# Performance work log

Measured on AMD Instinct MI355X. Metric: run time of the kernel, lower is better.

Reference implementation:

```python
import jax, jax.numpy as jnp
import numpy as np

DIM = 1024
HEADS = 16
HEAD_DIM = DIM // HEADS
B, N = 2, 2048


def setup_inputs() -> dict:
    key = jax.random.key(0)
    k1, k2, k3, k4 = jax.random.split(key, 4)
    scale = 1.0 / np.sqrt(DIM)
    return {
        "x": jax.random.normal(k1, (B, N, DIM), dtype=jnp.float32),
        "w_qkv": jax.random.normal(k2, (DIM, 3 * DIM), dtype=jnp.float32) * scale,
        "w_out": jax.random.normal(k3, (DIM, DIM), dtype=jnp.float32) * scale,
        "b_out": jax.random.normal(k4, (DIM,), dtype=jnp.float32) * 0.01,
    }


def reference(x, w_qkv, w_out, b_out):
    b, n, c = x.shape
    h, d = HEADS, c // HEADS
    sm_scale = d ** -0.5
    qkv = x @ w_qkv  # [b, n, 3c]
    q, k, v = jnp.split(qkv, 3, axis=-1)
    # [b, n, c] -> [b, h, n, d]
    q = q.reshape(b, n, h, d).transpose(0, 2, 1, 3)
    k = k.reshape(b, n, h, d).transpose(0, 2, 1, 3)
    v = v.reshape(b, n, h, d).transpose(0, 2, 1, 3)
    dots = jnp.einsum("bhqd,bhkd->bhqk", q, k) * sm_scale
    attn = jax.nn.softmax(dots, axis=-1)
    out = jnp.einsum("bhqk,bhkd->bhqd", attn, v)
    out = out.transpose(0, 2, 1, 3).reshape(b, n, c)
    return out @ w_out + b_out
```

## Files before the change

### kernel.cpp

```cpp
#include <hip/hip_runtime.h>
#include <hip/hip_bf16.h>

typedef __attribute__((ext_vector_type(8))) short bf16x8;
typedef __attribute__((ext_vector_type(4))) float f32x4;

#define B_    2
#define N_    2048
#define DIM_  1024
#define H_    16
#define D_    64
#define BH_   32
#define QSC   0.18033688f

static __device__ __forceinline__ void gload_lds16(const void* g, void* l) {
  __builtin_amdgcn_global_load_lds((const __attribute__((address_space(1))) void*)g,
                                   (__attribute__((address_space(3))) void*)l, 16, 0, 0);
}

__global__ __launch_bounds__(256) void cvt_x_kernel(const float* __restrict__ in,
                                                    __hip_bfloat16* __restrict__ out, int n4) {
  int i = blockIdx.x * 256 + threadIdx.x;
  if (i >= n4) return;
  float4 v = reinterpret_cast<const float4*>(in)[i];
  union { __hip_bfloat16 h[4]; uint2 u; } cv;
  cv.h[0] = __float2bfloat16(v.x);
  cv.h[1] = __float2bfloat16(v.y);
  cv.h[2] = __float2bfloat16(v.z);
  cv.h[3] = __float2bfloat16(v.w);
  reinterpret_cast<uint2*>(out)[i] = cv.u;
}

__global__ __launch_bounds__(256) void tconv_kernel(const float* __restrict__ in,
                                                    __hip_bfloat16* __restrict__ out,
                                                    int R, int C) {
  __shared__ float tile[64][65];
  const int c0 = blockIdx.x * 64, r0 = blockIdx.y * 64;
  const int t = threadIdx.x;
#pragma unroll
  for (int i = 0; i < 16; ++i) {
    int idx = i * 256 + t;
    int r = idx >> 6, c = idx & 63;
    tile[r][c] = in[(size_t)(r0 + r) * C + (c0 + c)];
  }
  __syncthreads();
#pragma unroll
  for (int i = 0; i < 16; ++i) {
    int idx = i * 256 + t;
    int rr = idx >> 6, cc = idx & 63;
    out[(size_t)(c0 + rr) * R + (r0 + cc)] = __float2bfloat16(tile[cc][rr]);
  }
}

__global__ __launch_bounds__(256) void gemm_qkv_kernel(const __hip_bfloat16* __restrict__ A,
                                                       const __hip_bfloat16* __restrict__ Bt,
                                                       __hip_bfloat16* __restrict__ Qw,
                                                       __hip_bfloat16* __restrict__ Kw,
                                                       __hip_bfloat16* __restrict__ Vt) {
  constexpr int K = 1024;
  __shared__ __align__(16) __hip_bfloat16 As[128 * 32];
  __shared__ __align__(16) __hip_bfloat16 Bs[128 * 32];
  const int t = threadIdx.x, w = t >> 6, lane = t & 63;
  const int l16 = lane & 15, kg = lane >> 4;
  const int m0 = blockIdx.y * 128, n0 = blockIdx.x * 128;
  const int wm = w >> 1, wn = w & 1;

  f32x4 acc[4][4];
#pragma unroll
  for (int i = 0; i < 4; ++i)
#pragma unroll
    for (int j = 0; j < 4; ++j) acc[i][j] = {0.f, 0.f, 0.f, 0.f};

  const int srow = w * 16 + (lane >> 2);
  const int scol = (lane & 3) * 8;
  const __hip_bfloat16* gA = A + (size_t)(m0 + srow) * K + scol;
  const __hip_bfloat16* gB = Bt + (size_t)(n0 + srow) * K + scol;
  char* lA = (char*)As + w * 1024;
  char* lB = (char*)Bs + w * 1024;

  for (int k0 = 0; k0 < K; k0 += 32) {
    __syncthreads();
    gload_lds16(gA + k0, lA);
    gload_lds16(gA + (size_t)64 * K + k0, lA + 4096);
    gload_lds16(gB + k0, lB);
    gload_lds16(gB + (size_t)64 * K + k0, lB + 4096);
    __syncthreads();
    bf16x8 a[4], b[4];
#pragma unroll
    for (int i = 0; i < 4; ++i)
      a[i] = *reinterpret_cast<const bf16x8*>(&As[(wm * 64 + i * 16 + l16) * 32 + kg * 8]);
#pragma unroll
    for (int j = 0; j < 4; ++j)
      b[j] = *reinterpret_cast<const bf16x8*>(&Bs[(wn * 64 + j * 16 + l16) * 32 + kg * 8]);
#pragma unroll
    for (int i = 0; i < 4; ++i)
#pragma unroll
      for (int j = 0; j < 4; ++j)
        acc[i][j] = __builtin_amdgcn_mfma_f32_16x16x32_bf16(a[i], b[j], acc[i][j], 0, 0, 0);
  }

#pragma unroll
  for (int j = 0; j < 4; ++j) {
    const int n = n0 + wn * 64 + j * 16 + l16;
    const int which = n >> 10, nn = n & 1023;
    const int h = nn >> 6, d = nn & 63;
#pragma unroll
    for (int i = 0; i < 4; ++i) {
      const int m = m0 + wm * 64 + i * 16 + kg * 4;
      const int bb = m >> 11, tt = m & 2047;
      if (which == 2) {
        union { __hip_bfloat16 hh[4]; unsigned long long u; } pv;
#pragma unroll
        for (int r = 0; r < 4; ++r) pv.hh[r] = __float2bfloat16(acc[i][j][r]);
        *reinterpret_cast<unsigned long long*>(
            &Vt[((size_t)(bb * H_ + h) * D_ + d) * N_ + tt]) = pv.u;
      } else {
        __hip_bfloat16* dst = (which == 0) ? Qw : Kw;
        const float sc = (which == 0) ? QSC : 1.0f;
#pragma unroll
        for (int r = 0; r < 4; ++r)
          dst[((size_t)(bb * H_ + h) * N_ + tt + r) * D_ + d] = __float2bfloat16(acc[i][j][r] * sc);
      }
    }
  }
}

__global__ __launch_bounds__(256) void gemm_out_kernel(const __hip_bfloat16* __restrict__ A,
                                                       const __hip_bfloat16* __restrict__ Bt,
                                                       const float* __restrict__ bo,
                                                       float* __restrict__ out) {
  constexpr int K = 1024;
  __shared__ __align__(16) __hip_bfloat16 As[128 * 32];
  __shared__ __align__(16) __hip_bfloat16 Bs[128 * 32];
  const int t = threadIdx.x, w = t >> 6, lane = t & 63;
  const int l16 = lane & 15, kg = lane >> 4;
  const int m0 = blockIdx.y * 128, n0 = blockIdx.x * 128;
  const int wm = w >> 1, wn = w & 1;

  f32x4 acc[4][4];
#pragma unroll
  for (int i = 0; i < 4; ++i)
#pragma unroll
    for (int j = 0; j < 4; ++j) acc[i][j] = {0.f, 0.f, 0.f, 0.f};

  const int srow = w * 16 + (lane >> 2);
  const int scol = (lane & 3) * 8;
  const __hip_bfloat16* gA = A + (size_t)(m0 + srow) * K + scol;
  const __hip_bfloat16* gB = Bt + (size_t)(n0 + srow) * K + scol;
  char* lA = (char*)As + w * 1024;
  char* lB = (char*)Bs + w * 1024;

  for (int k0 = 0; k0 < K; k0 += 32) {
    __syncthreads();
    gload_lds16(gA + k0, lA);
    gload_lds16(gA + (size_t)64 * K + k0, lA + 4096);
    gload_lds16(gB + k0, lB);
    gload_lds16(gB + (size_t)64 * K + k0, lB + 4096);
    __syncthreads();
    bf16x8 a[4], b[4];
#pragma unroll
    for (int i = 0; i < 4; ++i)
      a[i] = *reinterpret_cast<const bf16x8*>(&As[(wm * 64 + i * 16 + l16) * 32 + kg * 8]);
#pragma unroll
    for (int j = 0; j < 4; ++j)
      b[j] = *reinterpret_cast<const bf16x8*>(&Bs[(wn * 64 + j * 16 + l16) * 32 + kg * 8]);
#pragma unroll
    for (int i = 0; i < 4; ++i)
#pragma unroll
      for (int j = 0; j < 4; ++j)
        acc[i][j] = __builtin_amdgcn_mfma_f32_16x16x32_bf16(a[i], b[j], acc[i][j], 0, 0, 0);
  }

#pragma unroll
  for (int j = 0; j < 4; ++j) {
    const int n = n0 + wn * 64 + j * 16 + l16;
    const float bias = bo[n];
#pragma unroll
    for (int i = 0; i < 4; ++i) {
#pragma unroll
      for (int r = 0; r < 4; ++r) {
        const int m = m0 + wm * 64 + i * 16 + kg * 4 + r;
        out[(size_t)m * 1024 + n] = acc[i][j][r] + bias;
      }
    }
  }
}

__global__ __launch_bounds__(512) void attn_kernel(const __hip_bfloat16* __restrict__ Q,
                                                   const __hip_bfloat16* __restrict__ K,
                                                   const __hip_bfloat16* __restrict__ Vt,
                                                   __hip_bfloat16* __restrict__ O) {
  __shared__ __align__(16) __hip_bfloat16 Ks[2][64 * 64];
  __shared__ __align__(16) __hip_bfloat16 Vs[2][64 * 64];
  __shared__ __align__(16) __hip_bfloat16 Plds[8][16][64];
  const int bh = blockIdx.y;
  const int q0 = blockIdx.x * 128;
  const int t = threadIdx.x, w = t >> 6, lane = t & 63;
  const int l16 = lane & 15, kg = lane >> 4;
  const int b = bh >> 4, h = bh & 15;

  const __hip_bfloat16* Kbh = K + (size_t)bh * N_ * D_;
  const __hip_bfloat16* Vbh = Vt + (size_t)bh * D_ * N_;

  const int crow = t >> 3, cb = t & 7;
  const int csw = cb ^ (crow & 7);
  const size_t offK = (size_t)crow * D_ + csw * 8;
  const size_t offV = (size_t)crow * N_ + csw * 8;

  const __hip_bfloat16* Qp = Q + ((size_t)bh * N_ + q0 + w * 16 + l16) * D_ + kg * 8;
  const bf16x8 qf0 = *reinterpret_cast<const bf16x8*>(Qp);
  const bf16x8 qf1 = *reinterpret_cast<const bf16x8*>(Qp + 32);

  bf16x8 ones;
#pragma unroll
  for (int i = 0; i < 8; ++i) ones[i] = (short)0x3F80;

  f32x4 oaccS = {0.f, 0.f, 0.f, 0.f};
  f32x4 oacc[4];
#pragma unroll
  for (int dn = 0; dn < 4; ++dn) oacc[dn] = {0.f, 0.f, 0.f, 0.f};

#define STAGE(bufi, kv)                                                          \
  do {                                                                           \
    gload_lds16(Kbh + (size_t)(kv) * D_ + offK, (char*)Ks[bufi] + w * 1024);     \
    gload_lds16(Vbh + (kv) + offV,              (char*)Vs[bufi] + w * 1024);     \
  } while (0)

  STAGE(0, 0);
  asm volatile("s_waitcnt vmcnt(0)" ::: "memory");
  __builtin_amdgcn_s_barrier();

#pragma unroll 1
  for (int it = 0; it < N_ / 64; ++it) {
    const int buf = it & 1;
    if (it + 1 < N_ / 64) STAGE(buf ^ 1, (it + 1) * 64);

    const char* Kb = (const char*)Ks[buf];
    const char* Vb = (const char*)Vs[buf];

    f32x4 s[4];
#pragma unroll
    for (int kt = 0; kt < 4; ++kt) s[kt] = {0.f, 0.f, 0.f, 0.f};
    __builtin_amdgcn_s_setprio(1);
#pragma unroll
    for (int kt = 0; kt < 4; ++kt) {
      const int row = kt * 16 + l16;
      const int rsw = (row & 7) << 4;
      const bf16x8 k0 = *reinterpret_cast<const bf16x8*>(Kb + row * 128 + ((kg << 4) ^ rsw));
      const bf16x8 k1 = *reinterpret_cast<const bf16x8*>(Kb + row * 128 + (((4 + kg) << 4) ^ rsw));
      s[kt] = __builtin_amdgcn_mfma_f32_16x16x32_bf16(k0, qf0, s[kt], 0, 0, 0);
      s[kt] = __builtin_amdgcn_mfma_f32_16x16x32_bf16(k1, qf1, s[kt], 0, 0, 0);
    }
    __builtin_amdgcn_s_setprio(0);

    const int xm3 = (l16 & 7) << 3;
#pragma unroll
    for (int kt = 0; kt < 4; ++kt) {
      union { __hip_bfloat16 hh[4]; unsigned long long u; } pk;
#pragma unroll
      for (int r = 0; r < 4; ++r) pk.hh[r] = __float2bfloat16(__builtin_amdgcn_exp2f(s[kt][r]));
      *reinterpret_cast<unsigned long long*>(&Plds[w][l16][(16 * kt + 4 * kg) ^ xm3]) = pk.u;
    }

    __builtin_amdgcn_s_setprio(1);
#pragma unroll
    for (int kk = 0; kk < 2; ++kk) {
      const bf16x8 pa = *reinterpret_cast<const bf16x8*>(
          &Plds[w][l16][(kk * 32 + kg * 8) ^ xm3]);
      oaccS = __builtin_amdgcn_mfma_f32_16x16x32_bf16(pa, ones, oaccS, 0, 0, 0);
#pragma unroll
      for (int dn = 0; dn < 4; ++dn) {
        const int vrow = dn * 16 + l16;
        const int vsw = (vrow & 7) << 4;
        const bf16x8 vf = *reinterpret_cast<const bf16x8*>(
            Vb + vrow * 128 + ((kk * 64 + kg * 16) ^ vsw));
        oacc[dn] = __builtin_amdgcn_mfma_f32_16x16x32_bf16(pa, vf, oacc[dn], 0, 0, 0);
      }
    }
    __builtin_amdgcn_s_setprio(0);

    asm volatile("s_waitcnt vmcnt(0)" ::: "memory");
    __builtin_amdgcn_s_barrier();
  }
#undef STAGE

  float inv[4];
#pragma unroll
  for (int r = 0; r < 4; ++r) inv[r] = 1.0f / oaccS[r];
  __hip_bfloat16* Ob = O + ((size_t)b * N_ + q0 + w * 16) * DIM_ + h * D_;
#pragma unroll
  for (int dn = 0; dn < 4; ++dn)
#pragma unroll
    for (int r = 0; r < 4; ++r)
      Ob[(size_t)(kg * 4 + r) * DIM_ + dn * 16 + l16] = __float2bfloat16(oacc[dn][r] * inv[r]);
}

extern "C" void kernel_launch(void* const* d_in, const int* in_sizes, int n_in,
                              void* d_out, int out_size, void* d_ws, size_t ws_size,
                              hipStream_t stream) {
  const float* x = (const float*)d_in[0];
  const float* w_qkv = (const float*)d_in[1];
  const float* w_out = (const float*)d_in[2];
  const float* b_out = (const float*)d_in[3];
  float* out = (float*)d_out;

  __hip_bfloat16* ws = (__hip_bfloat16*)d_ws;
  __hip_bfloat16* xb = ws;
  __hip_bfloat16* wqkT = xb + (size_t)4096 * 1024;
  __hip_bfloat16* woT = wqkT + (size_t)3072 * 1024;
  __hip_bfloat16* Qw = woT + (size_t)1024 * 1024;
  __hip_bfloat16* Kw = Qw + (size_t)BH_ * N_ * D_;
  __hip_bfloat16* Vt = Kw + (size_t)BH_ * N_ * D_;
  __hip_bfloat16* Ow = Vt + (size_t)BH_ * N_ * D_;

  cvt_x_kernel<<<4096, 256, 0, stream>>>(x, xb, 4096 * 1024 / 4);
  tconv_kernel<<<dim3(48, 16), 256, 0, stream>>>(w_qkv, wqkT, 1024, 3072);
  tconv_kernel<<<dim3(16, 16), 256, 0, stream>>>(w_out, woT, 1024, 1024);
  gemm_qkv_kernel<<<dim3(24, 32), 256, 0, stream>>>(xb, wqkT, Qw, Kw, Vt);
  attn_kernel<<<dim3(16, 32), 512, 0, stream>>>(Qw, Kw, Vt, Ow);
  gemm_out_kernel<<<dim3(8, 32), 256, 0, stream>>>(Ow, woT, b_out, out);
}
```

Before: 120.0 us.

## Rewrite attention with 32x32 MFMA, register-resident P, and triple-buffered K/V

The attention kernel moves from 16x16x32 to 32x32x16 MFMA tiles, so each wave handles 32 query rows and each block 256 rows, which halves the grid. The softmax probabilities are passed from the QK^T output layout into the PV operand layout through lane shuffles instead of an LDS round trip. The row-sum now comes from scalar adds of the exp values rather than an extra MFMA against ones. K/V staging becomes a three-deep ring with vmcnt(2) waits and one barrier per iteration. This raises register pressure (launch_bounds 512,2) and the halved grid of 256 blocks may leave some compute units underused.

```diff
diff --git a/kernel.cpp b/kernel.cpp
--- a/kernel.cpp
+++ b/kernel.cpp
@@ -3,6 +3,7 @@
 
 typedef __attribute__((ext_vector_type(8))) short bf16x8;
 typedef __attribute__((ext_vector_type(4))) float f32x4;
+typedef __attribute__((ext_vector_type(16))) float f32x16;
 
 #define B_    2
 #define N_    2048
@@ -185,17 +186,16 @@
   }
 }
 
-__global__ __launch_bounds__(512) void attn_kernel(const __hip_bfloat16* __restrict__ Q,
-                                                   const __hip_bfloat16* __restrict__ K,
-                                                   const __hip_bfloat16* __restrict__ Vt,
-                                                   __hip_bfloat16* __restrict__ O) {
-  __shared__ __align__(16) __hip_bfloat16 Ks[2][64 * 64];
-  __shared__ __align__(16) __hip_bfloat16 Vs[2][64 * 64];
-  __shared__ __align__(16) __hip_bfloat16 Plds[8][16][64];
+__global__ __launch_bounds__(512, 2) void attn_kernel(const __hip_bfloat16* __restrict__ Q,
+                                                      const __hip_bfloat16* __restrict__ K,
+                                                      const __hip_bfloat16* __restrict__ Vt,
+                                                      __hip_bfloat16* __restrict__ O) {
+  __shared__ __align__(16) __hip_bfloat16 Ks[3][64 * 64];
+  __shared__ __align__(16) __hip_bfloat16 Vs[3][64 * 64];
   const int bh = blockIdx.y;
-  const int q0 = blockIdx.x * 128;
+  const int q0 = blockIdx.x * 256;
   const int t = threadIdx.x, w = t >> 6, lane = t & 63;
-  const int l16 = lane & 15, kg = lane >> 4;
+  const int l32 = lane & 31, hi = lane >> 5;
   const int b = bh >> 4, h = bh & 15;
 
   const __hip_bfloat16* Kbh = K + (size_t)bh * N_ * D_;
@@ -206,92 +206,110 @@
   const size_t offK = (size_t)crow * D_ + csw * 8;
   const size_t offV = (size_t)crow * N_ + csw * 8;
 
-  const __hip_bfloat16* Qp = Q + ((size_t)bh * N_ + q0 + w * 16 + l16) * D_ + kg * 8;
-  const bf16x8 qf0 = *reinterpret_cast<const bf16x8*>(Qp);
-  const bf16x8 qf1 = *reinterpret_cast<const bf16x8*>(Qp + 32);
-
-  bf16x8 ones;
-#pragma unroll
-  for (int i = 0; i < 8; ++i) ones[i] = (short)0x3F80;
-
-  f32x4 oaccS = {0.f, 0.f, 0.f, 0.f};
-  f32x4 oacc[4];
-#pragma unroll
-  for (int dn = 0; dn < 4; ++dn) oacc[dn] = {0.f, 0.f, 0.f, 0.f};
-
-#define STAGE(bufi, kv)                                                          \
-  do {                                                                           \
-    gload_lds16(Kbh + (size_t)(kv) * D_ + offK, (char*)Ks[bufi] + w * 1024);     \
-    gload_lds16(Vbh + (kv) + offV,              (char*)Vs[bufi] + w * 1024);     \
+  const __hip_bfloat16* Qrow = Q + ((size_t)bh * N_ + q0 + w * 32 + l32) * D_ + hi * 8;
+  bf16x8 qf[4];
+#pragma unroll
+  for (int ks = 0; ks < 4; ++ks)
+    qf[ks] = *reinterpret_cast<const bf16x8*>(Qrow + 16 * ks);
+
+  f32x16 o0, o1;
+#pragma unroll
+  for (int i = 0; i < 16; ++i) { o0[i] = 0.f; o1[i] = 0.f; }
+  float dacc = 0.f;
+
+#define STAGE(bufi, kv)                                                        \
+  do {                                                                         \
+    gload_lds16(Kbh + (size_t)(kv) * D_ + offK, (char*)Ks[bufi] + w * 1024);   \
+    gload_lds16(Vbh + (kv) + offV,              (char*)Vs[bufi] + w * 1024);   \
   } while (0)
 
   STAGE(0, 0);
-  asm volatile("s_waitcnt vmcnt(0)" ::: "memory");
-  __builtin_amdgcn_s_barrier();
+  STAGE(1, 64);
 
 #pragma unroll 1
   for (int it = 0; it < N_ / 64; ++it) {
-    const int buf = it & 1;
-    if (it + 1 < N_ / 64) STAGE(buf ^ 1, (it + 1) * 64);
-
-    const char* Kb = (const char*)Ks[buf];
-    const char* Vb = (const char*)Vs[buf];
-
-    f32x4 s[4];
-#pragma unroll
-    for (int kt = 0; kt < 4; ++kt) s[kt] = {0.f, 0.f, 0.f, 0.f};
+    asm volatile("s_waitcnt vmcnt(2)" ::: "memory");
+    __builtin_amdgcn_s_barrier();
+    if (it + 2 < N_ / 64) STAGE((it + 2) % 3, (it + 2) * 64);
+
+    const char* Kb = (const char*)Ks[it % 3];
+    const char* Vb = (const char*)Vs[it % 3];
+
+    f32x16 s0, s1;
+#pragma unroll
+    for (int i = 0; i < 16; ++i) { s0[i] = 0.f; s1[i] = 0.f; }
     __builtin_amdgcn_s_setprio(1);
 #pragma unroll
-    for (int kt = 0; kt < 4; ++kt) {
-      const int row = kt * 16 + l16;
-      const int rsw = (row & 7) << 4;
-      const bf16x8 k0 = *reinterpret_cast<const bf16x8*>(Kb + row * 128 + ((kg << 4) ^ rsw));
-      const bf16x8 k1 = *reinterpret_cast<const bf16x8*>(Kb + row * 128 + (((4 + kg) << 4) ^ rsw));
-      s[kt] = __builtin_amdgcn_mfma_f32_16x16x32_bf16(k0, qf0, s[kt], 0, 0, 0);
-      s[kt] = __builtin_amdgcn_mfma_f32_16x16x32_bf16(k1, qf1, s[kt], 0, 0, 0);
+    for (int ks = 0; ks < 4; ++ks) {
+      const int bsel = (((ks << 1) | hi) ^ (l32 & 7)) << 4;
+      const bf16x8 k0 = *reinterpret_cast<const bf16x8*>(Kb + l32 * 128 + bsel);
+      const bf16x8 k1 = *reinterpret_cast<const bf16x8*>(Kb + (32 + l32) * 128 + bsel);
+      s0 = __builtin_amdgcn_mfma_f32_32x32x16_bf16(k0, qf[ks], s0, 0, 0, 0);
+      s1 = __builtin_amdgcn_mfma_f32_32x32x16_bf16(k1, qf[ks], s1, 0, 0, 0);
     }
     __builtin_amdgcn_s_setprio(0);
 
-    const int xm3 = (l16 & 7) << 3;
-#pragma unroll
-    for (int kt = 0; kt < 4; ++kt) {
-      union { __hip_bfloat16 hh[4]; unsigned long long u; } pk;
-#pragma unroll
-      for (int r = 0; r < 4; ++r) pk.hh[r] = __float2bfloat16(__builtin_amdgcn_exp2f(s[kt][r]));
-      *reinterpret_cast<unsigned long long*>(&Plds[w][l16][(16 * kt + 4 * kg) ^ xm3]) = pk.u;
-    }
+    unsigned u[2][4][2];
+    float ds = 0.f;
+#pragma unroll
+    for (int kvb = 0; kvb < 2; ++kvb)
+#pragma unroll
+      for (int rq = 0; rq < 4; ++rq)
+#pragma unroll
+        for (int i = 0; i < 2; ++i) {
+          const float pa_ = __builtin_amdgcn_exp2f(kvb ? s1[4 * rq + 2 * i] : s0[4 * rq + 2 * i]);
+          const float pb_ = __builtin_amdgcn_exp2f(kvb ? s1[4 * rq + 2 * i + 1] : s0[4 * rq + 2 * i + 1]);
+          ds += pa_ + pb_;
+          union { __hip_bfloat162 h2; unsigned uu; } cv;
+          cv.h2 = __float22bfloat162_rn(make_float2(pa_, pb_));
+          u[kvb][rq][i] = cv.uu;
+        }
+    dacc += ds;
+
+    bf16x8 pf[4];
+#pragma unroll
+    for (int cbk = 0; cbk < 2; ++cbk)
+#pragma unroll
+      for (int cl = 0; cl < 2; ++cl) {
+        unsigned wlo[2], whl[2];
+#pragma unroll
+        for (int i = 0; i < 2; ++i) {
+          const unsigned push = hi ? u[cbk][2 * cl][i] : u[cbk][2 * cl + 1][i];
+          const unsigned xr = (unsigned)__shfl_xor((int)push, 32);
+          wlo[i] = hi ? xr : u[cbk][2 * cl][i];
+          whl[i] = hi ? u[cbk][2 * cl + 1][i] : xr;
+        }
+        union { unsigned uu[4]; bf16x8 v; } pk;
+        pk.uu[0] = wlo[0]; pk.uu[1] = wlo[1]; pk.uu[2] = whl[0]; pk.uu[3] = whl[1];
+        pf[2 * cbk + cl] = pk.v;
+      }
 
     __builtin_amdgcn_s_setprio(1);
 #pragma unroll
-    for (int kk = 0; kk < 2; ++kk) {
-      const bf16x8 pa = *reinterpret_cast<const bf16x8*>(
-          &Plds[w][l16][(kk * 32 + kg * 8) ^ xm3]);
-      oaccS = __builtin_amdgcn_mfma_f32_16x16x32_bf16(pa, ones, oaccS, 0, 0, 0);
-#pragma unroll
-      for (int dn = 0; dn < 4; ++dn) {
-        const int vrow = dn * 16 + l16;
-        const int vsw = (vrow & 7) << 4;
-        const bf16x8 vf = *reinterpret_cast<const bf16x8*>(
-            Vb + vrow * 128 + ((kk * 64 + kg * 16) ^ vsw));
-        oacc[dn] = __builtin_amdgcn_mfma_f32_16x16x32_bf16(pa, vf, oacc[dn], 0, 0, 0);
-      }
+    for (int c = 0; c < 4; ++c) {
+      const int bsel = (((c << 1) | hi) ^ (l32 & 7)) << 4;
+      const bf16x8 v0 = *reinterpret_cast<const bf16x8*>(Vb + l32 * 128 + bsel);
+      const bf16x8 v1 = *reinterpret_cast<const bf16x8*>(Vb + (32 + l32) * 128 + bsel);
+      o0 = __builtin_amdgcn_mfma_f32_32x32x16_bf16(v0, pf[c], o0, 0, 0, 0);
+      o1 = __builtin_amdgcn_mfma_f32_32x32x16_bf16(v1, pf[c], o1, 0, 0, 0);
     }
     __builtin_amdgcn_s_setprio(0);
-
-    asm volatile("s_waitcnt vmcnt(0)" ::: "memory");
-    __builtin_amdgcn_s_barrier();
   }
 #undef STAGE
 
-  float inv[4];
-#pragma unroll
-  for (int r = 0; r < 4; ++r) inv[r] = 1.0f / oaccS[r];
-  __hip_bfloat16* Ob = O + ((size_t)b * N_ + q0 + w * 16) * DIM_ + h * D_;
-#pragma unroll
-  for (int dn = 0; dn < 4; ++dn)
-#pragma unroll
-    for (int r = 0; r < 4; ++r)
-      Ob[(size_t)(kg * 4 + r) * DIM_ + dn * 16 + l16] = __float2bfloat16(oacc[dn][r] * inv[r]);
+  const float den = dacc + __shfl_xor(dacc, 32);
+  const float inv = 1.0f / den;
+  __hip_bfloat16* Ob = O + ((size_t)b * N_ + q0 + w * 32 + l32) * DIM_ + h * D_;
+#pragma unroll
+  for (int dblk = 0; dblk < 2; ++dblk)
+#pragma unroll
+    for (int rq = 0; rq < 4; ++rq) {
+      union { __hip_bfloat16 hh[4]; unsigned long long uu; } pk;
+#pragma unroll
+      for (int j = 0; j < 4; ++j)
+        pk.hh[j] = __float2bfloat16((dblk ? o1[4 * rq + j] : o0[4 * rq + j]) * inv);
+      *reinterpret_cast<unsigned long long*>(Ob + dblk * 32 + rq * 8 + hi * 4) = pk.uu;
+    }
 }
 
 extern "C" void kernel_launch(void* const* d_in, const int* in_sizes, int n_in,
@@ -316,6 +334,6 @@
   tconv_kernel<<<dim3(48, 16), 256, 0, stream>>>(w_qkv, wqkT, 1024, 3072);
   tconv_kernel<<<dim3(16, 16), 256, 0, stream>>>(w_out, woT, 1024, 1024);
   gemm_qkv_kernel<<<dim3(24, 32), 256, 0, stream>>>(xb, wqkT, Qw, Kw, Vt);
-  attn_kernel<<<dim3(16, 32), 512, 0, stream>>>(Qw, Kw, Vt, Ow);
+  attn_kernel<<<dim3(8, 32), 512, 0, stream>>>(Qw, Kw, Vt, Ow);
   gemm_out_kernel<<<dim3(8, 32), 256, 0, stream>>>(Ow, woT, b_out, out);
 }
```

New measurement: 135.6 us. +12.9%, slower.

## Merge prep kernels into one launch and use K=64 swizzled LDS tiles in GEMMs

Applied to the files above, without the earlier changes.

The x conversion and both weight transpose-converts now run as a single prep kernel launch. Two launches and their gaps go away. Both GEMMs now stage 64-wide K slices with an XOR-swizzled LDS layout, which halves the barrier pairs per K and is meant to avoid LDS bank conflicts on the fragment reads. LDS use per block doubles, which may lower occupancy.

```diff
diff --git a/kernel.cpp b/kernel.cpp
--- a/kernel.cpp
+++ b/kernel.cpp
@@ -17,25 +17,37 @@
                                    (__attribute__((address_space(3))) void*)l, 16, 0, 0);
 }
 
-__global__ __launch_bounds__(256) void cvt_x_kernel(const float* __restrict__ in,
-                                                    __hip_bfloat16* __restrict__ out, int n4) {
-  int i = blockIdx.x * 256 + threadIdx.x;
-  if (i >= n4) return;
-  float4 v = reinterpret_cast<const float4*>(in)[i];
-  union { __hip_bfloat16 h[4]; uint2 u; } cv;
-  cv.h[0] = __float2bfloat16(v.x);
-  cv.h[1] = __float2bfloat16(v.y);
-  cv.h[2] = __float2bfloat16(v.z);
-  cv.h[3] = __float2bfloat16(v.w);
-  reinterpret_cast<uint2*>(out)[i] = cv.u;
-}
-
-__global__ __launch_bounds__(256) void tconv_kernel(const float* __restrict__ in,
-                                                    __hip_bfloat16* __restrict__ out,
-                                                    int R, int C) {
+__global__ __launch_bounds__(256) void prep_kernel(const float* __restrict__ x,
+                                                   const float* __restrict__ w_qkv,
+                                                   const float* __restrict__ w_out,
+                                                   __hip_bfloat16* __restrict__ xb,
+                                                   __hip_bfloat16* __restrict__ wqkT,
+                                                   __hip_bfloat16* __restrict__ woT) {
   __shared__ float tile[64][65];
-  const int c0 = blockIdx.x * 64, r0 = blockIdx.y * 64;
-  const int t = threadIdx.x;
+  const int bid = blockIdx.x, t = threadIdx.x;
+  if (bid < 4096) {
+    const int i = bid * 256 + t;
+    float4 v = reinterpret_cast<const float4*>(x)[i];
+    union { __hip_bfloat16 h[4]; uint2 u; } cv;
+    cv.h[0] = __float2bfloat16(v.x);
+    cv.h[1] = __float2bfloat16(v.y);
+    cv.h[2] = __float2bfloat16(v.z);
+    cv.h[3] = __float2bfloat16(v.w);
+    reinterpret_cast<uint2*>(xb)[i] = cv.u;
+    return;
+  }
+  const float* in;
+  __hip_bfloat16* out;
+  int R, C, c0, r0;
+  if (bid < 4096 + 768) {
+    const int bx = bid - 4096;
+    in = w_qkv; out = wqkT; R = 1024; C = 3072;
+    c0 = (bx % 48) * 64; r0 = (bx / 48) * 64;
+  } else {
+    const int bx = bid - 4096 - 768;
+    in = w_out; out = woT; R = 1024; C = 1024;
+    c0 = (bx % 16) * 64; r0 = (bx / 16) * 64;
+  }
 #pragma unroll
   for (int i = 0; i < 16; ++i) {
     int idx = i * 256 + t;
@@ -50,53 +62,57 @@
     out[(size_t)(c0 + rr) * R + (r0 + cc)] = __float2bfloat16(tile[cc][rr]);
   }
 }
+
+#define GEMM_CORE(A_, Bt_)                                                               \
+  constexpr int K = 1024;                                                                \
+  __shared__ __align__(16) __hip_bfloat16 As[128 * 64];                                  \
+  __shared__ __align__(16) __hip_bfloat16 Bs[128 * 64];                                  \
+  const int t = threadIdx.x, w = t >> 6, lane = t & 63;                                  \
+  const int l16 = lane & 15, kg = lane >> 4;                                             \
+  const int m0 = blockIdx.y * 128, n0 = blockIdx.x * 128;                                \
+  const int wm = w >> 1, wn = w & 1;                                                     \
+  f32x4 acc[4][4];                                                                       \
+  _Pragma("unroll") for (int i = 0; i < 4; ++i)                                          \
+    _Pragma("unroll") for (int j = 0; j < 4; ++j) acc[i][j] = {0.f, 0.f, 0.f, 0.f};      \
+                \
+  size_t srcA[4], srcB[4];                                                               \
+  _Pragma("unroll") for (int i = 0; i < 4; ++i) {                                        \
+    const int c = 256 * i + t;                                                           \
+    const int row = c >> 3, jsw = (c & 7) ^ (row & 7);                                   \
+    srcA[i] = (size_t)(m0 + row) * K + jsw * 8;                                          \
+    srcB[i] = (size_t)(n0 + row) * K + jsw * 8;                                          \
+  }                                                                                      \
+  for (int k0 = 0; k0 < K; k0 += 64) {                                                   \
+    __syncthreads();                                                                     \
+    _Pragma("unroll") for (int i = 0; i < 4; ++i) {                                      \
+      gload_lds16(A_ + srcA[i] + k0, (char*)As + 4096 * i + 1024 * w);                   \
+      gload_lds16(Bt_ + srcB[i] + k0, (char*)Bs + 4096 * i + 1024 * w);                  \
+    }                                                                                    \
+    __syncthreads();                                                                     \
+    _Pragma("unroll") for (int kk = 0; kk < 2; ++kk) {                                   \
+      bf16x8 a[4], b[4];                                                                 \
+      _Pragma("unroll") for (int i = 0; i < 4; ++i) {                                    \
+        const int row = wm * 64 + i * 16 + l16;                                          \
+        const int jsw = ((kk << 2) | kg) ^ (row & 7);                                    \
+        a[i] = *reinterpret_cast<const bf16x8*>((const char*)As + row * 128 + jsw * 16); \
+      }                                                                                  \
+      _Pragma("unroll") for (int j = 0; j < 4; ++j) {                                    \
+        const int row = wn * 64 + j * 16 + l16;                                          \
+        const int jsw = ((kk << 2) | kg) ^ (row & 7);                                    \
+        b[j] = *reinterpret_cast<const bf16x8*>((const char*)Bs + row * 128 + jsw * 16); \
+      }                                                                                  \
+      _Pragma("unroll") for (int i = 0; i < 4; ++i)                                      \
+        _Pragma("unroll") for (int j = 0; j < 4; ++j)                                    \
+          acc[i][j] = __builtin_amdgcn_mfma_f32_16x16x32_bf16(a[i], b[j], acc[i][j], 0, 0, 0); \
+    }                                                                                    \
+  }
 
 __global__ __launch_bounds__(256) void gemm_qkv_kernel(const __hip_bfloat16* __restrict__ A,
                                                        const __hip_bfloat16* __restrict__ Bt,
                                                        __hip_bfloat16* __restrict__ Qw,
                                                        __hip_bfloat16* __restrict__ Kw,
                                                        __hip_bfloat16* __restrict__ Vt) {
-  constexpr int K = 1024;
-  __shared__ __align__(16) __hip_bfloat16 As[128 * 32];
-  __shared__ __align__(16) __hip_bfloat16 Bs[128 * 32];
-  const int t = threadIdx.x, w = t >> 6, lane = t & 63;
-  const int l16 = lane & 15, kg = lane >> 4;
-  const int m0 = blockIdx.y * 128, n0 = blockIdx.x * 128;
-  const int wm = w >> 1, wn = w & 1;
-
-  f32x4 acc[4][4];
-#pragma unroll
-  for (int i = 0; i < 4; ++i)
-#pragma unroll
-    for (int j = 0; j < 4; ++j) acc[i][j] = {0.f, 0.f, 0.f, 0.f};
-
-  const int srow = w * 16 + (lane >> 2);
-  const int scol = (lane & 3) * 8;
-  const __hip_bfloat16* gA = A + (size_t)(m0 + srow) * K + scol;
-  const __hip_bfloat16* gB = Bt + (size_t)(n0 + srow) * K + scol;
-  char* lA = (char*)As + w * 1024;
-  char* lB = (char*)Bs + w * 1024;
-
-  for (int k0 = 0; k0 < K; k0 += 32) {
-    __syncthreads();
-    gload_lds16(gA + k0, lA);
-    gload_lds16(gA + (size_t)64 * K + k0, lA + 4096);
-    gload_lds16(gB + k0, lB);
-    gload_lds16(gB + (size_t)64 * K + k0, lB + 4096);
-    __syncthreads();
-    bf16x8 a[4], b[4];
-#pragma unroll
-    for (int i = 0; i < 4; ++i)
-      a[i] = *reinterpret_cast<const bf16x8*>(&As[(wm * 64 + i * 16 + l16) * 32 + kg * 8]);
-#pragma unroll
-    for (int j = 0; j < 4; ++j)
-      b[j] = *reinterpret_cast<const bf16x8*>(&Bs[(wn * 64 + j * 16 + l16) * 32 + kg * 8]);
-#pragma unroll
-    for (int i = 0; i < 4; ++i)
-#pragma unroll
-      for (int j = 0; j < 4; ++j)
-        acc[i][j] = __builtin_amdgcn_mfma_f32_16x16x32_bf16(a[i], b[j], acc[i][j], 0, 0, 0);
-  }
+  GEMM_CORE(A, Bt)
 
 #pragma unroll
   for (int j = 0; j < 4; ++j) {
@@ -128,47 +144,7 @@
                                                        const __hip_bfloat16* __restrict__ Bt,
                                                        const float* __restrict__ bo,
                                                        float* __restrict__ out) {
-  constexpr int K = 1024;
-  __shared__ __align__(16) __hip_bfloat16 As[128 * 32];
-  __shared__ __align__(16) __hip_bfloat16 Bs[128 * 32];
-  const int t = threadIdx.x, w = t >> 6, lane = t & 63;
-  const int l16 = lane & 15, kg = lane >> 4;
-  const int m0 = blockIdx.y * 128, n0 = blockIdx.x * 128;
-  const int wm = w >> 1, wn = w & 1;
-
-  f32x4 acc[4][4];
-#pragma unroll
-  for (int i = 0; i < 4; ++i)
-#pragma unroll
-    for (int j = 0; j < 4; ++j) acc[i][j] = {0.f, 0.f, 0.f, 0.f};
-
-  const int srow = w * 16 + (lane >> 2);
-  const int scol = (lane & 3) * 8;
-  const __hip_bfloat16* gA = A + (size_t)(m0 + srow) * K + scol;
-  const __hip_bfloat16* gB = Bt + (size_t)(n0 + srow) * K + scol;
-  char* lA = (char*)As + w * 1024;
-  char* lB = (char*)Bs + w * 1024;
-
-  for (int k0 = 0; k0 < K; k0 += 32) {
-    __syncthreads();
-    gload_lds16(gA + k0, lA);
-    gload_lds16(gA + (size_t)64 * K + k0, lA + 4096);
-    gload_lds16(gB + k0, lB);
-    gload_lds16(gB + (size_t)64 * K + k0, lB + 4096);
-    __syncthreads();
-    bf16x8 a[4], b[4];
-#pragma unroll
-    for (int i = 0; i < 4; ++i)
-      a[i] = *reinterpret_cast<const bf16x8*>(&As[(wm * 64 + i * 16 + l16) * 32 + kg * 8]);
-#pragma unroll
-    for (int j = 0; j < 4; ++j)
-      b[j] = *reinterpret_cast<const bf16x8*>(&Bs[(wn * 64 + j * 16 + l16) * 32 + kg * 8]);
-#pragma unroll
-    for (int i = 0; i < 4; ++i)
-#pragma unroll
-      for (int j = 0; j < 4; ++j)
-        acc[i][j] = __builtin_amdgcn_mfma_f32_16x16x32_bf16(a[i], b[j], acc[i][j], 0, 0, 0);
-  }
+  GEMM_CORE(A, Bt)
 
 #pragma unroll
   for (int j = 0; j < 4; ++j) {
@@ -312,9 +288,7 @@
   __hip_bfloat16* Vt = Kw + (size_t)BH_ * N_ * D_;
   __hip_bfloat16* Ow = Vt + (size_t)BH_ * N_ * D_;
 
-  cvt_x_kernel<<<4096, 256, 0, stream>>>(x, xb, 4096 * 1024 / 4);
-  tconv_kernel<<<dim3(48, 16), 256, 0, stream>>>(w_qkv, wqkT, 1024, 3072);
-  tconv_kernel<<<dim3(16, 16), 256, 0, stream>>>(w_out, woT, 1024, 1024);
+  prep_kernel<<<5120, 256, 0, stream>>>(x, w_qkv, w_out, xb, wqkT, woT);
   gemm_qkv_kernel<<<dim3(24, 32), 256, 0, stream>>>(xb, wqkT, Qw, Kw, Vt);
   attn_kernel<<<dim3(16, 32), 512, 0, stream>>>(Qw, Kw, Vt, Ow);
   gemm_out_kernel<<<dim3(8, 32), 256, 0, stream>>>(Ow, woT, b_out, out);
```

After: 122.6 us. 2.1% more time.
